# Kernel tuning notes

Measured on AMD Instinct MI355X. Metric: run time of the kernel, lower is better.

The kernel has to match this reference:

```python
import jax, jax.numpy as jnp
import numpy as np

N_NODES = 100000
N_EDGES = 3200000
NUM_GRAPHS = 512


def _glorot(key, shape):
    fan_in, fan_out = shape[0], shape[1]
    lim = float(np.sqrt(6.0 / (fan_in + fan_out)))
    return jax.random.uniform(key, shape, jnp.float32, -lim, lim)


def setup_inputs() -> dict:
    key = jax.random.key(0)
    ks = jax.random.split(key, 12)
    x = jax.random.normal(ks[0], (N_NODES, 3), jnp.float32)
    edge_index = jax.random.randint(ks[1], (2, N_EDGES), 0, N_NODES, jnp.int64)
    batch = jnp.sort(jax.random.randint(ks[2], (N_NODES,), 0, NUM_GRAPHS, jnp.int64))
    return {
        'x': x,
        'edge_index': edge_index,
        'batch': batch,
        'W1': _glorot(ks[3], (3, 32)), 'b1': jnp.zeros((32,), jnp.float32),
        'W2': _glorot(ks[4], (32, 64)), 'b2': jnp.zeros((64,), jnp.float32),
        'W3': _glorot(ks[5], (64, 64)), 'b3': jnp.zeros((64,), jnp.float32),
        'lW1': _glorot(ks[6], (64, 32)), 'lb1': jnp.zeros((32,), jnp.float32),
        'lW2': _glorot(ks[7], (32, 5)), 'lb2': jnp.zeros((5,), jnp.float32),
    }


def gcn_conv(x, src, dst, W, b, n):
    # PyG GCNConv: add self-loops, symmetric deg^{-1/2} normalization,
    # linear transform then gather-scale-scatter aggregation.
    loop = jnp.arange(n, dtype=src.dtype)
    s = jnp.concatenate([src, loop])
    d = jnp.concatenate([dst, loop])
    deg = jax.ops.segment_sum(jnp.ones_like(d, dtype=x.dtype), d, num_segments=n)
    dinv = jnp.where(deg > 0, jax.lax.rsqrt(deg), 0.0)
    norm = dinv[s] * dinv[d]  # [E+N]
    h = x @ W                 # [N, out]
    out = jax.ops.segment_sum(h[s] * norm[:, None], d, num_segments=n)
    return out + b


def reference(x, edge_index, batch, W1, b1, W2, b2, W3, b3, lW1, lb1, lW2, lb2):
    src, dst = edge_index[0], edge_index[1]
    n = x.shape[0]
    h = jax.nn.relu(gcn_conv(x, src, dst, W1, b1, n))
    h = jax.nn.relu(gcn_conv(h, src, dst, W2, b2, n))
    h = gcn_conv(h, src, dst, W3, b3, n)
    pooled = jax.ops.segment_sum(h, batch, num_segments=NUM_GRAPHS)  # [G, 64]
    z = jax.nn.relu(pooled @ lW1 + lb1)
    z = z @ lW2 + lb2
    # original applies log_softmax over dim=0 (the graph axis)
    return jax.nn.log_softmax(z, axis=0)
```

## Files before the change

### kernel.cpp

```cpp
#include <hip/hip_runtime.h>
#include <hip/hip_fp16.h>

#define N_GRAPHS 512
#define NB 1563
#define KNODE 64
#define CAP 3072
#define EPW 8192


__global__ void k_part(const int4* __restrict__ src4, const int4* __restrict__ dst4,
                       int* __restrict__ gCnt, unsigned* __restrict__ ebuf, int E4) {
    __shared__ unsigned pos[NB];
    __shared__ int dstc[EPW];
    int t = threadIdx.x;
    int e0 = blockIdx.x * (EPW / 4);
    int cnt4 = E4 - e0 < EPW / 4 ? E4 - e0 : EPW / 4;
    for (int i = t; i < NB; i += 256) pos[i] = 0;
    __syncthreads();
    for (int i = t; i < cnt4; i += 256) {
        int4 d = dst4[e0 + i];
        dstc[4 * i + 0] = d.x; dstc[4 * i + 1] = d.y;
        dstc[4 * i + 2] = d.z; dstc[4 * i + 3] = d.w;
        atomicAdd(&pos[d.x >> 6], 1u);
        atomicAdd(&pos[d.y >> 6], 1u);
        atomicAdd(&pos[d.z >> 6], 1u);
        atomicAdd(&pos[d.w >> 6], 1u);
    }
    __syncthreads();
    for (int b = t; b < NB; b += 256) {
        unsigned c = pos[b];
        unsigned base = c ? (unsigned)atomicAdd(&gCnt[b], (int)c) : 0u;
        pos[b] = (unsigned)b * CAP + base;
    }
    __syncthreads();
    for (int i = t; i < cnt4; i += 256) {
        int4 s = src4[e0 + i];
#pragma unroll
        for (int q = 0; q < 4; ++q) {
            int d = dstc[4 * i + q];
            int sv = q == 0 ? s.x : q == 1 ? s.y : q == 2 ? s.z : s.w;
            int bkt = d >> 6;
            unsigned p = atomicAdd(&pos[bkt], 1u);
            if (p < (unsigned)(bkt + 1) * CAP)
                ebuf[p] = (unsigned)sv | ((unsigned)(d & 63) << 20);
        }
    }
}


__global__ void k_csr(unsigned* __restrict__ ebuf, const int* __restrict__ gCnt,
                      int2* __restrict__ rows, float* __restrict__ dinv, int n) {
    __shared__ unsigned ec[CAP];
    __shared__ int deg[KNODE];
    __shared__ int pfx[KNODE];
    int b = blockIdx.x, t = threadIdx.x;
    int cnt = gCnt[b];
    if (cnt > CAP) cnt = CAP;
    if (t < KNODE) deg[t] = 0;
    __syncthreads();
    unsigned* eb = ebuf + (size_t)b * CAP;
    for (int i = t; i < cnt; i += 256) {
        unsigned p = eb[i];
        ec[i] = p;
        atomicAdd(&deg[p >> 20], 1);
    }
    __syncthreads();
    if (t == 0) {
        int a = 0;
        for (int i = 0; i < KNODE; ++i) { pfx[i] = a; a += deg[i]; }
    }
    __syncthreads();
    if (t < KNODE) {
        int node = b * KNODE + t;
        if (node < n) {
            rows[node] = make_int2(b * CAP + pfx[t], deg[t]);
            dinv[node] = rsqrtf((float)(deg[t] + 1));
        }
    }
    if (t < KNODE) deg[t] = pfx[t];
    __syncthreads();
    for (int i = t; i < cnt; i += 256) {
        unsigned p = ec[i];
        int pp = atomicAdd(&deg[p >> 20], 1);
        eb[pp] = p & 0xFFFFFu;
    }
}


__global__ void k_pre1(const float* __restrict__ x, const float* __restrict__ dinv,
                       float4* __restrict__ ts0, int n) {
    int i = blockIdx.x * 256 + threadIdx.x;
    if (i >= n) return;
    float d = dinv[i];
    ts0[i] = make_float4(d * x[3 * i], d * x[3 * i + 1], d * x[3 * i + 2], 0.f);
}


__global__ void k_agg1(const float4* __restrict__ ts0, const unsigned* __restrict__ esrc,
                       const int2* __restrict__ rows, const float* __restrict__ dinv,
                       float4* __restrict__ o1, int n) {
    int node = blockIdx.x * 256 + threadIdx.x;
    if (node >= n) return;
    int2 rc = rows[node];
    int s0 = rc.x, deg = rc.y;
    float4 a = ts0[node];
    int e = 0;
    for (; e + 4 <= deg; e += 4) {
        unsigned i0 = esrc[s0 + e + 0];
        unsigned i1 = esrc[s0 + e + 1];
        unsigned i2 = esrc[s0 + e + 2];
        unsigned i3 = esrc[s0 + e + 3];
        float4 v0 = ts0[i0], v1 = ts0[i1], v2 = ts0[i2], v3 = ts0[i3];
        a.x += v0.x + v1.x + v2.x + v3.x;
        a.y += v0.y + v1.y + v2.y + v3.y;
        a.z += v0.z + v1.z + v2.z + v3.z;
    }
    for (; e < deg; ++e) {
        float4 v = ts0[esrc[s0 + e]];
        a.x += v.x; a.y += v.y; a.z += v.z;
    }
    float d = dinv[node];
    o1[node] = make_float4(d * a.x, d * a.y, d * a.z, 0.f);
}


__global__ void k_t1(const float4* __restrict__ o1, const float* __restrict__ W1,
                     const float* __restrict__ b1, const float* __restrict__ dinv,
                     uint4* __restrict__ ts1, int n) {
    __shared__ float sW[96];
    __shared__ float sb[32];
    int t = threadIdx.x;
    if (t < 96) sW[t] = W1[t];
    if (t < 32) sb[t] = b1[t];
    __syncthreads();
    int ln = t >> 2, c = t & 3;
    int node = blockIdx.x * 64 + ln;
    if (node >= n) return;
    float4 o = o1[node];
    float d = dinv[node];
    float r[8];
#pragma unroll
    for (int k = 0; k < 8; ++k) {
        int j = c * 8 + k;
        float h = o.x * sW[j] + o.y * sW[32 + j] + o.z * sW[64 + j] + sb[j];
        r[k] = fmaxf(h, 0.f) * d;
    }
    __half2 h0 = __floats2half2_rn(r[0], r[1]);
    __half2 h1 = __floats2half2_rn(r[2], r[3]);
    __half2 h2 = __floats2half2_rn(r[4], r[5]);
    __half2 h3 = __floats2half2_rn(r[6], r[7]);
    uint4 w;
    w.x = *(unsigned*)&h0; w.y = *(unsigned*)&h1;
    w.z = *(unsigned*)&h2; w.w = *(unsigned*)&h3;
    ts1[(size_t)node * 4 + c] = w;
}


template <int NSLICE>
__global__ void k_aggW(const uint4* __restrict__ ts, const unsigned* __restrict__ ebuf,
                       const int* __restrict__ gCnt, const int2* __restrict__ rows,
                       const float* __restrict__ dinv, uint4* __restrict__ out, int n) {
    __shared__ unsigned eidx[CAP];
    __shared__ int cursor;
    int i = blockIdx.x;
    int b, slice;
    if (NSLICE == 1) {
        b = i; slice = 0;
    } else {
        int xcd = i & 7;
        slice = xcd & 1;
        b = (i >> 3) * 4 + (xcd >> 1);
    }
    if (b >= NB) return;
    int t = threadIdx.x;
    int cnt = gCnt[b];
    if (cnt > CAP) cnt = CAP;
    int bBase = b * CAP;
    const uint4* ebuf4 = (const uint4*)(ebuf + bBase);
    int cnt4 = (cnt + 3) >> 2;
    for (int k = t; k < cnt4; k += 128) ((uint4*)eidx)[k] = ebuf4[k];
    if (t == 0) cursor = 0;
    __syncthreads();

    const uint4* tss = ts + (size_t)slice * n * 4;
    int lane = t & 3;
    for (;;) {
        int my;
        if (lane == 0) my = atomicAdd(&cursor, 1);
        my = __shfl(my, 0, 4);
        if (my >= KNODE) break;
        int node = b * KNODE + my;
        if (node >= n) continue;
        int2 rc = rows[node];
        int ls = rc.x - bBase;
        int deg = rc.y;
        float2 a0, a1, a2, a3;
        {
            uint4 sv = tss[(size_t)node * 4 + lane];
            a0 = __half22float2(*(__half2*)&sv.x);
            a1 = __half22float2(*(__half2*)&sv.y);
            a2 = __half22float2(*(__half2*)&sv.z);
            a3 = __half22float2(*(__half2*)&sv.w);
        }
        int e = 0;
        for (; e + 4 <= deg; e += 4) {
            unsigned s0 = eidx[ls + e + 0];
            unsigned s1 = eidx[ls + e + 1];
            unsigned s2 = eidx[ls + e + 2];
            unsigned s3 = eidx[ls + e + 3];
            uint4 v0 = tss[(size_t)s0 * 4 + lane];
            uint4 v1 = tss[(size_t)s1 * 4 + lane];
            uint4 v2 = tss[(size_t)s2 * 4 + lane];
            uint4 v3 = tss[(size_t)s3 * 4 + lane];
            float2 f;
            f = __half22float2(*(__half2*)&v0.x); a0.x += f.x; a0.y += f.y;
            f = __half22float2(*(__half2*)&v0.y); a1.x += f.x; a1.y += f.y;
            f = __half22float2(*(__half2*)&v0.z); a2.x += f.x; a2.y += f.y;
            f = __half22float2(*(__half2*)&v0.w); a3.x += f.x; a3.y += f.y;
            f = __half22float2(*(__half2*)&v1.x); a0.x += f.x; a0.y += f.y;
            f = __half22float2(*(__half2*)&v1.y); a1.x += f.x; a1.y += f.y;
            f = __half22float2(*(__half2*)&v1.z); a2.x += f.x; a2.y += f.y;
            f = __half22float2(*(__half2*)&v1.w); a3.x += f.x; a3.y += f.y;
            f = __half22float2(*(__half2*)&v2.x); a0.x += f.x; a0.y += f.y;
            f = __half22float2(*(__half2*)&v2.y); a1.x += f.x; a1.y += f.y;
            f = __half22float2(*(__half2*)&v2.z); a2.x += f.x; a2.y += f.y;
            f = __half22float2(*(__half2*)&v2.w); a3.x += f.x; a3.y += f.y;
            f = __half22float2(*(__half2*)&v3.x); a0.x += f.x; a0.y += f.y;
            f = __half22float2(*(__half2*)&v3.y); a1.x += f.x; a1.y += f.y;
            f = __half22float2(*(__half2*)&v3.z); a2.x += f.x; a2.y += f.y;
            f = __half22float2(*(__half2*)&v3.w); a3.x += f.x; a3.y += f.y;
        }
        for (; e < deg; ++e) {
            unsigned s = eidx[ls + e];
            uint4 v = tss[(size_t)s * 4 + lane];
            float2 f;
            f = __half22float2(*(__half2*)&v.x); a0.x += f.x; a0.y += f.y;
            f = __half22float2(*(__half2*)&v.y); a1.x += f.x; a1.y += f.y;
            f = __half22float2(*(__half2*)&v.z); a2.x += f.x; a2.y += f.y;
            f = __half22float2(*(__half2*)&v.w); a3.x += f.x; a3.y += f.y;
        }
        float dd = dinv[node];
        __half2 o0 = __floats2half2_rn(dd * a0.x, dd * a0.y);
        __half2 o1 = __floats2half2_rn(dd * a1.x, dd * a1.y);
        __half2 o2 = __floats2half2_rn(dd * a2.x, dd * a2.y);
        __half2 o3 = __floats2half2_rn(dd * a3.x, dd * a3.y);
        uint4 w;
        w.x = *(unsigned*)&o0; w.y = *(unsigned*)&o1;
        w.z = *(unsigned*)&o2; w.w = *(unsigned*)&o3;
        out[(size_t)node * (NSLICE * 4) + slice * 4 + lane] = w;
    }
}


__global__ void k_t2(const uint4* __restrict__ o2, const float* __restrict__ W2,
                     const float* __restrict__ b2, const float* __restrict__ dinv,
                     uint4* __restrict__ ts2, int n) {
    __shared__ uint4 sO[128];
    __shared__ float sW[32 * 64];
    __shared__ float sb[64];
    int t = threadIdx.x;
    for (int i = t; i < 32 * 64; i += 256) sW[i] = W2[i];
    if (t < 64) sb[t] = b2[t];
    int node0 = blockIdx.x * 32;
    if (t < 128) {
        int nd = node0 + (t >> 2);
        sO[t] = (nd < n) ? o2[(size_t)node0 * 4 + t] : make_uint4(0, 0, 0, 0);
    }
    __syncthreads();
    int ln = t >> 3, c = t & 7;
    int node = node0 + ln;
    if (node >= n) return;
    const __half2* sOh = (const __half2*)sO;
    float acc[8];
#pragma unroll
    for (int k = 0; k < 8; ++k) acc[k] = sb[c * 8 + k];
#pragma unroll
    for (int i2 = 0; i2 < 16; ++i2) {
        float2 av = __half22float2(sOh[ln * 16 + i2]);
        const float* w0 = &sW[(2 * i2) * 64 + c * 8];
        const float* w1 = &sW[(2 * i2 + 1) * 64 + c * 8];
#pragma unroll
        for (int k = 0; k < 8; ++k) acc[k] += av.x * w0[k] + av.y * w1[k];
    }
    float d = dinv[node];
    float r[8];
#pragma unroll
    for (int k = 0; k < 8; ++k) r[k] = fmaxf(acc[k], 0.f) * d;
    __half2 h0 = __floats2half2_rn(r[0], r[1]);
    __half2 h1 = __floats2half2_rn(r[2], r[3]);
    __half2 h2 = __floats2half2_rn(r[4], r[5]);
    __half2 h3 = __floats2half2_rn(r[6], r[7]);
    uint4 w;
    w.x = *(unsigned*)&h0; w.y = *(unsigned*)&h1;
    w.z = *(unsigned*)&h2; w.w = *(unsigned*)&h3;
    ts2[((size_t)(c >> 2) * n + node) * 4 + (c & 3)] = w;
}


__global__ void k_pool(const __half2* __restrict__ h, const int* __restrict__ batch,
                       float* __restrict__ pooled, float* __restrict__ cntf, int n) {
    const int NBK = 32;
    int lane = threadIdx.x & 31;
    int sub = threadIdx.x >> 5;
    int n0 = (blockIdx.x * 8 + sub) * NBK;
    if (n0 >= n) return;
    int nend = n0 + NBK < n ? n0 + NBK : n;
    float2 acc = make_float2(0.f, 0.f);
    float rc = 0.f;
    int gcur = batch[n0];
    for (int i = n0; i < nend; ++i) {
        int g = batch[i];
        if (g != gcur) {
            atomicAdd(&pooled[gcur * 64 + 2 * lane], acc.x);
            atomicAdd(&pooled[gcur * 64 + 2 * lane + 1], acc.y);
            if (lane == 0) atomicAdd(&cntf[gcur], rc);
            acc = make_float2(0.f, 0.f);
            rc = 0.f;
            gcur = g;
        }
        float2 v = __half22float2(h[(size_t)i * 32 + lane]);
        acc.x += v.x;
        acc.y += v.y;
        rc += 1.f;
    }
    atomicAdd(&pooled[gcur * 64 + 2 * lane], acc.x);
    atomicAdd(&pooled[gcur * 64 + 2 * lane + 1], acc.y);
    if (lane == 0) atomicAdd(&cntf[gcur], rc);
}


#define GPB 4
__global__ void k_z(const float* __restrict__ P, const float* __restrict__ cntf,
                    const float* __restrict__ W3, const float* __restrict__ b3,
                    const float* __restrict__ lW1, const float* __restrict__ lb1,
                    const float* __restrict__ lW2, const float* __restrict__ lb2,
                    float* __restrict__ z) {
    __shared__ float sW3[64 * 64];
    __shared__ float sW1[64 * 32];
    __shared__ float sW2[32 * 5];
    __shared__ float sb3[64], sb1[32], sb2[5];
    __shared__ float sP[GPB][64];
    __shared__ float sH[GPB][64];
    __shared__ float sT[GPB][32];
    int t = threadIdx.x;
    for (int i = t; i < 64 * 64; i += 256) sW3[i] = W3[i];
    for (int i = t; i < 64 * 32; i += 256) sW1[i] = lW1[i];
    for (int i = t; i < 32 * 5; i += 256) sW2[i] = lW2[i];
    if (t < 64) sb3[t] = b3[t];
    if (t < 32) sb1[t] = lb1[t];
    if (t < 5) sb2[t] = lb2[t];
    int g0 = blockIdx.x * GPB;
    for (int i = t; i < GPB * 64; i += 256) sP[i >> 6][i & 63] = P[(size_t)g0 * 64 + i];
    __syncthreads();
    int lg = t >> 6;
    int j = t & 63;
    int g = g0 + lg;
    float cg = cntf[g];
    float a = cg * sb3[j];
#pragma unroll 8
    for (int i = 0; i < 64; ++i) a += sP[lg][i] * sW3[i * 64 + j];
    sH[lg][j] = a;
    __syncthreads();
    if (j < 32) {
        float a2 = sb1[j];
#pragma unroll 8
        for (int i = 0; i < 64; ++i) a2 += sH[lg][i] * sW1[i * 32 + j];
        sT[lg][j] = fmaxf(a2, 0.f);
    }
    __syncthreads();
    if (j < 5) {
        float a3 = sb2[j];
#pragma unroll
        for (int i = 0; i < 32; ++i) a3 += sT[lg][i] * sW2[i * 5 + j];
        z[g * 5 + j] = a3;
    }
}


__global__ void k_lsm(const float* __restrict__ z, float* __restrict__ out) {
    __shared__ float red[512];
    int g = threadIdx.x;
#pragma unroll
    for (int c = 0; c < 5; ++c) {
        float v = z[g * 5 + c];
        red[g] = v;
        __syncthreads();
        for (int off = 256; off > 0; off >>= 1) {
            if (g < off) red[g] = fmaxf(red[g], red[g + off]);
            __syncthreads();
        }
        float m = red[0];
        __syncthreads();
        red[g] = expf(v - m);
        __syncthreads();
        for (int off = 256; off > 0; off >>= 1) {
            if (g < off) red[g] += red[g + off];
            __syncthreads();
        }
        float lse = m + logf(red[0]);
        __syncthreads();
        out[g * 5 + c] = v - lse;
    }
}


extern "C" void kernel_launch(void* const* d_in, const int* in_sizes, int n_in,
                              void* d_out, int out_size, void* d_ws, size_t ws_size,
                              hipStream_t stream) {
    const float* x   = (const float*)d_in[0];
    const int* ei    = (const int*)d_in[1];
    const int* batch = (const int*)d_in[2];
    const float* W1  = (const float*)d_in[3];
    const float* b1  = (const float*)d_in[4];
    const float* W2  = (const float*)d_in[5];
    const float* b2  = (const float*)d_in[6];
    const float* W3  = (const float*)d_in[7];
    const float* b3  = (const float*)d_in[8];
    const float* lW1 = (const float*)d_in[9];
    const float* lb1 = (const float*)d_in[10];
    const float* lW2 = (const float*)d_in[11];
    const float* lb2 = (const float*)d_in[12];

    const int N = in_sizes[0] / 3;
    const int E = in_sizes[1] / 2;
    const int* src = ei;
    const int* dst = ei + E;

    char* ws = (char*)d_ws;
    size_t off = 0;
    auto alloc = [&](size_t bytes) -> void* {
        void* p = ws + off;
        off = (off + bytes + 255) & ~(size_t)255;
        return p;
    };

    int*      gCnt    = (int*)alloc((size_t)NB * 4);
    float*    dinv    = (float*)alloc((size_t)N * 4);
    int2*     rows    = (int2*)alloc((size_t)N * 8);
    unsigned* ebuf    = (unsigned*)alloc((size_t)NB * CAP * 4);
    float4*   ts0     = (float4*)alloc((size_t)N * 16);
    float4*   o1      = (float4*)alloc((size_t)N * 16);
    uint4*    ts1     = (uint4*)alloc((size_t)N * 4 * 16);
    uint4*    o2      = (uint4*)alloc((size_t)N * 4 * 16);
    uint4*    ts2     = (uint4*)alloc((size_t)N * 8 * 16);
    uint4*    o3      = (uint4*)alloc((size_t)N * 8 * 16);
    float*    pooledP = (float*)alloc((size_t)N_GRAPHS * 64 * 4);
    float*    cntf    = (float*)alloc((size_t)N_GRAPHS * 4);
    float*    zbuf    = (float*)alloc((size_t)N_GRAPHS * 5 * 4);

    hipMemsetAsync(gCnt, 0, (size_t)NB * 4, stream);
    hipMemsetAsync(pooledP, 0, (size_t)N_GRAPHS * 64 * 4, stream);
    hipMemsetAsync(cntf, 0, (size_t)N_GRAPHS * 4, stream);

    int nPartWg = (E + EPW - 1) / EPW;
    k_part<<<nPartWg, 256, 0, stream>>>((const int4*)src, (const int4*)dst, gCnt, ebuf, E / 4);
    k_csr<<<NB, 256, 0, stream>>>(ebuf, gCnt, rows, dinv, N);

    k_pre1<<<(N + 255) / 256, 256, 0, stream>>>(x, dinv, ts0, N);
    k_agg1<<<(N + 255) / 256, 256, 0, stream>>>(ts0, ebuf, rows, dinv, o1, N);
    k_t1<<<(N + 63) / 64, 256, 0, stream>>>(o1, W1, b1, dinv, ts1, N);

    k_aggW<1><<<NB, 128, 0, stream>>>(ts1, ebuf, gCnt, rows, dinv, o2, N);
    k_t2<<<(N + 31) / 32, 256, 0, stream>>>(o2, W2, b2, dinv, ts2, N);

    k_aggW<2><<<8 * ((NB + 3) / 4), 128, 0, stream>>>(ts2, ebuf, gCnt, rows, dinv, o3, N);

    k_pool<<<(N + 8 * 32 - 1) / (8 * 32), 256, 0, stream>>>((const __half2*)o3, batch,
                                                            pooledP, cntf, N);
    k_z<<<N_GRAPHS / GPB, 256, 0, stream>>>(pooledP, cntf, W3, b3, lW1, lb1, lW2, lb2, zbuf);
    k_lsm<<<1, 512, 0, stream>>>(zbuf, (float*)d_out);
}
```

Baseline: 245.9 us.

## Replace global-atomic bucket partition with per-chunk sort plus transposed offset table

The edge partition step no longer reserves bucket space with global atomics. Each chunk sorts its edges locally by bucket and writes them contiguously, and it records per-bucket start and count in a table. That table is transposed so each CSR block can prefix-sum the chunk offsets and gather its edges from every chunk. Workspace buffers are also aliased to reduce the memory footprint. The aim is to remove contended global atomics and scattered writes, at the cost of an extra transpose kernel and a serial per-chunk copy loop in the CSR kernel.

```diff
diff --git a/kernel.cpp b/kernel.cpp
--- a/kernel.cpp
+++ b/kernel.cpp
@@ -6,83 +6,171 @@
 #define KNODE 64
 #define CAP 3072
 #define EPW 8192
-
-
-__global__ void k_part(const int4* __restrict__ src4, const int4* __restrict__ dst4,
-                       int* __restrict__ gCnt, unsigned* __restrict__ ebuf, int E4) {
-    __shared__ unsigned pos[NB];
+#define NWMAX 400
+
+
+__global__ void k_part2(const int4* __restrict__ src4, const int4* __restrict__ dst4,
+                        unsigned* __restrict__ ebuf2, unsigned* __restrict__ P, int E, int nw) {
     __shared__ int dstc[EPW];
-    int t = threadIdx.x;
-    int e0 = blockIdx.x * (EPW / 4);
-    int cnt4 = E4 - e0 < EPW / 4 ? E4 - e0 : EPW / 4;
-    for (int i = t; i < NB; i += 256) pos[i] = 0;
-    __syncthreads();
+    __shared__ unsigned hist[NB];
+    __shared__ unsigned tsum[256];
+    int w = blockIdx.x, t = threadIdx.x;
+    int e0 = w * EPW;
+    int cnt = E - e0 < EPW ? E - e0 : EPW;
+    int cnt4 = cnt >> 2;
+    for (int i = t; i < NB; i += 256) hist[i] = 0;
+    __syncthreads();
+    const int4* d4 = dst4 + (e0 >> 2);
+    const int4* s4 = src4 + (e0 >> 2);
     for (int i = t; i < cnt4; i += 256) {
-        int4 d = dst4[e0 + i];
+        int4 d = d4[i];
         dstc[4 * i + 0] = d.x; dstc[4 * i + 1] = d.y;
         dstc[4 * i + 2] = d.z; dstc[4 * i + 3] = d.w;
-        atomicAdd(&pos[d.x >> 6], 1u);
-        atomicAdd(&pos[d.y >> 6], 1u);
-        atomicAdd(&pos[d.z >> 6], 1u);
-        atomicAdd(&pos[d.w >> 6], 1u);
-    }
-    __syncthreads();
-    for (int b = t; b < NB; b += 256) {
-        unsigned c = pos[b];
-        unsigned base = c ? (unsigned)atomicAdd(&gCnt[b], (int)c) : 0u;
-        pos[b] = (unsigned)b * CAP + base;
+        atomicAdd(&hist[d.x >> 6], 1u);
+        atomicAdd(&hist[d.y >> 6], 1u);
+        atomicAdd(&hist[d.z >> 6], 1u);
+        atomicAdd(&hist[d.w >> 6], 1u);
+    }
+    __syncthreads();
+    const int PT7 = 7;
+    unsigned loc[PT7];
+    int base = t * PT7;
+    unsigned s = 0;
+#pragma unroll
+    for (int k = 0; k < PT7; ++k) {
+        int idx = base + k;
+        unsigned v = (idx < NB) ? hist[idx] : 0u;
+        loc[k] = s;
+        s += v;
+    }
+    tsum[t] = s;
+    __syncthreads();
+    for (int off = 1; off < 256; off <<= 1) {
+        unsigned u = (t >= off) ? tsum[t - off] : 0u;
+        __syncthreads();
+        tsum[t] += u;
+        __syncthreads();
+    }
+    unsigned toff = tsum[t] - s;
+#pragma unroll
+    for (int k = 0; k < PT7; ++k) {
+        int idx = base + k;
+        if (idx < NB) {
+            unsigned cb = ((k < PT7 - 1) ? loc[k + 1] : s) - loc[k];
+            unsigned st = toff + loc[k];
+            P[(size_t)w * NB + idx] = (st << 16) | cb;
+        }
+    }
+    __syncthreads();
+#pragma unroll
+    for (int k = 0; k < PT7; ++k) {
+        int idx = base + k;
+        if (idx < NB) hist[idx] = toff + loc[k];
     }
     __syncthreads();
     for (int i = t; i < cnt4; i += 256) {
-        int4 s = src4[e0 + i];
+        int4 sv = s4[i];
 #pragma unroll
         for (int q = 0; q < 4; ++q) {
             int d = dstc[4 * i + q];
-            int sv = q == 0 ? s.x : q == 1 ? s.y : q == 2 ? s.z : s.w;
+            int svv = q == 0 ? sv.x : q == 1 ? sv.y : q == 2 ? sv.z : sv.w;
             int bkt = d >> 6;
-            unsigned p = atomicAdd(&pos[bkt], 1u);
-            if (p < (unsigned)(bkt + 1) * CAP)
-                ebuf[p] = (unsigned)sv | ((unsigned)(d & 63) << 20);
-        }
-    }
-}
-
-
-__global__ void k_csr(unsigned* __restrict__ ebuf, const int* __restrict__ gCnt,
-                      int2* __restrict__ rows, float* __restrict__ dinv, int n) {
+            unsigned pos = atomicAdd(&hist[bkt], 1u);
+            ebuf2[(size_t)e0 + pos] = (unsigned)svv | ((unsigned)(d & 63) << 20);
+        }
+    }
+}
+
+
+__global__ void kT(const unsigned* __restrict__ P, unsigned* __restrict__ PT, int nw) {
+    __shared__ unsigned tile[32][33];
+    int bw = blockIdx.x;
+    int bb = blockIdx.y;
+    int tx = threadIdx.x & 31, ty = threadIdx.x >> 5;
+#pragma unroll
+    for (int r = 0; r < 32; r += 8) {
+        int w = bw * 32 + ty + r;
+        int b = bb * 32 + tx;
+        tile[ty + r][tx] = (w < nw && b < NB) ? P[(size_t)w * NB + b] : 0u;
+    }
+    __syncthreads();
+#pragma unroll
+    for (int r = 0; r < 32; r += 8) {
+        int b = bb * 32 + ty + r;
+        int w = bw * 32 + tx;
+        if (b < NB && w < nw) PT[(size_t)b * nw + w] = tile[tx][ty + r];
+    }
+}
+
+
+__global__ void k_csr2(const unsigned* __restrict__ ebuf2, const unsigned* __restrict__ PT,
+                       unsigned* __restrict__ ebufF, int* __restrict__ gCnt,
+                       int2* __restrict__ rows, float* __restrict__ dinv, int n, int nw) {
     __shared__ unsigned ec[CAP];
-    __shared__ int deg[KNODE];
-    __shared__ int pfx[KNODE];
+    __shared__ unsigned info[NWMAX];
+    __shared__ unsigned coff[NWMAX];
+    __shared__ unsigned tsum[256];
+    __shared__ int bins[KNODE], pfx[KNODE];
     int b = blockIdx.x, t = threadIdx.x;
-    int cnt = gCnt[b];
-    if (cnt > CAP) cnt = CAP;
-    if (t < KNODE) deg[t] = 0;
-    __syncthreads();
-    unsigned* eb = ebuf + (size_t)b * CAP;
-    for (int i = t; i < cnt; i += 256) {
-        unsigned p = eb[i];
-        ec[i] = p;
-        atomicAdd(&deg[p >> 20], 1);
-    }
+    for (int w = t; w < nw; w += 256) info[w] = PT[(size_t)b * nw + w];
+    __syncthreads();
+    unsigned l0, l1, s = 0;
+    {
+        int i0 = t * 2, i1 = t * 2 + 1;
+        unsigned v0 = (i0 < nw) ? (info[i0] & 0xFFFFu) : 0u;
+        unsigned v1 = (i1 < nw) ? (info[i1] & 0xFFFFu) : 0u;
+        l0 = 0; l1 = v0; s = v0 + v1;
+    }
+    tsum[t] = s;
+    __syncthreads();
+    for (int off = 1; off < 256; off <<= 1) {
+        unsigned u = (t >= off) ? tsum[t - off] : 0u;
+        __syncthreads();
+        tsum[t] += u;
+        __syncthreads();
+    }
+    unsigned toff = tsum[t] - s;
+    {
+        int i0 = t * 2, i1 = t * 2 + 1;
+        if (i0 < nw) coff[i0] = toff + l0;
+        if (i1 < nw) coff[i1] = toff + l1;
+    }
+    __syncthreads();
+    int total = (int)tsum[255];
+    int cnt = total < CAP ? total : CAP;
+    if (t == 0) gCnt[b] = cnt;
+    for (int w = t; w < nw; w += 256) {
+        unsigned inf = info[w];
+        unsigned st = inf >> 16, c = inf & 0xFFFFu;
+        unsigned d0 = coff[w];
+        const unsigned* src = ebuf2 + (size_t)w * EPW + st;
+        for (unsigned k = 0; k < c; ++k) {
+            unsigned p = d0 + k;
+            if (p < (unsigned)CAP) ec[p] = src[k];
+        }
+    }
+    if (t < KNODE) bins[t] = 0;
+    __syncthreads();
+    for (int i = t; i < cnt; i += 256) atomicAdd(&bins[ec[i] >> 20], 1);
     __syncthreads();
     if (t == 0) {
         int a = 0;
-        for (int i = 0; i < KNODE; ++i) { pfx[i] = a; a += deg[i]; }
+        for (int i = 0; i < KNODE; ++i) { pfx[i] = a; a += bins[i]; }
     }
     __syncthreads();
     if (t < KNODE) {
         int node = b * KNODE + t;
         if (node < n) {
-            rows[node] = make_int2(b * CAP + pfx[t], deg[t]);
-            dinv[node] = rsqrtf((float)(deg[t] + 1));
-        }
-    }
-    if (t < KNODE) deg[t] = pfx[t];
+            rows[node] = make_int2(b * CAP + pfx[t], bins[t]);
+            dinv[node] = rsqrtf((float)(bins[t] + 1));
+        }
+    }
+    if (t < KNODE) bins[t] = pfx[t];
     __syncthreads();
     for (int i = t; i < cnt; i += 256) {
         unsigned p = ec[i];
-        int pp = atomicAdd(&deg[p >> 20], 1);
-        eb[pp] = p & 0xFFFFFu;
+        int pp = atomicAdd(&bins[p >> 20], 1);
+        ebufF[(size_t)b * CAP + pp] = p & 0xFFFFFu;
     }
 }
 
@@ -425,6 +513,7 @@
     const int E = in_sizes[1] / 2;
     const int* src = ei;
     const int* dst = ei + E;
+    const int nw = (E + EPW - 1) / EPW;
 
     char* ws = (char*)d_ws;
     size_t off = 0;
@@ -437,33 +526,36 @@
     int*      gCnt    = (int*)alloc((size_t)NB * 4);
     float*    dinv    = (float*)alloc((size_t)N * 4);
     int2*     rows    = (int2*)alloc((size_t)N * 8);
-    unsigned* ebuf    = (unsigned*)alloc((size_t)NB * CAP * 4);
-    float4*   ts0     = (float4*)alloc((size_t)N * 16);
-    float4*   o1      = (float4*)alloc((size_t)N * 16);
+    unsigned* ebuf2   = (unsigned*)alloc((size_t)nw * EPW * 4);
+    unsigned* P       = (unsigned*)alloc((size_t)nw * NB * 4);
+    unsigned* PT      = (unsigned*)alloc((size_t)NB * nw * 4);
+    unsigned* ebufF   = (unsigned*)alloc((size_t)NB * CAP * 4);
     uint4*    ts1     = (uint4*)alloc((size_t)N * 4 * 16);
     uint4*    o2      = (uint4*)alloc((size_t)N * 4 * 16);
     uint4*    ts2     = (uint4*)alloc((size_t)N * 8 * 16);
-    uint4*    o3      = (uint4*)alloc((size_t)N * 8 * 16);
     float*    pooledP = (float*)alloc((size_t)N_GRAPHS * 64 * 4);
     float*    cntf    = (float*)alloc((size_t)N_GRAPHS * 4);
     float*    zbuf    = (float*)alloc((size_t)N_GRAPHS * 5 * 4);
-
-    hipMemsetAsync(gCnt, 0, (size_t)NB * 4, stream);
+    float4*   ts0     = (float4*)P;
+    float4*   o1      = (float4*)PT;
+    uint4*    o3      = (uint4*)ebuf2;
+
     hipMemsetAsync(pooledP, 0, (size_t)N_GRAPHS * 64 * 4, stream);
     hipMemsetAsync(cntf, 0, (size_t)N_GRAPHS * 4, stream);
 
-    int nPartWg = (E + EPW - 1) / EPW;
-    k_part<<<nPartWg, 256, 0, stream>>>((const int4*)src, (const int4*)dst, gCnt, ebuf, E / 4);
-    k_csr<<<NB, 256, 0, stream>>>(ebuf, gCnt, rows, dinv, N);
+    k_part2<<<nw, 256, 0, stream>>>((const int4*)src, (const int4*)dst, ebuf2, P, E, nw);
+    dim3 gT((nw + 31) / 32, (NB + 31) / 32);
+    kT<<<gT, 256, 0, stream>>>(P, PT, nw);
+    k_csr2<<<NB, 256, 0, stream>>>(ebuf2, PT, ebufF, gCnt, rows, dinv, N, nw);
 
     k_pre1<<<(N + 255) / 256, 256, 0, stream>>>(x, dinv, ts0, N);
-    k_agg1<<<(N + 255) / 256, 256, 0, stream>>>(ts0, ebuf, rows, dinv, o1, N);
+    k_agg1<<<(N + 255) / 256, 256, 0, stream>>>(ts0, ebufF, rows, dinv, o1, N);
     k_t1<<<(N + 63) / 64, 256, 0, stream>>>(o1, W1, b1, dinv, ts1, N);
 
-    k_aggW<1><<<NB, 128, 0, stream>>>(ts1, ebuf, gCnt, rows, dinv, o2, N);
+    k_aggW<1><<<NB, 128, 0, stream>>>(ts1, ebufF, gCnt, rows, dinv, o2, N);
     k_t2<<<(N + 31) / 32, 256, 0, stream>>>(o2, W2, b2, dinv, ts2, N);
 
-    k_aggW<2><<<8 * ((NB + 3) / 4), 128, 0, stream>>>(ts2, ebuf, gCnt, rows, dinv, o3, N);
+    k_aggW<2><<<8 * ((NB + 3) / 4), 128, 0, stream>>>(ts2, ebufF, gCnt, rows, dinv, o3, N);
 
     k_pool<<<(N + 8 * 32 - 1) / (8 * 32), 256, 0, stream>>>((const __half2*)o3, batch,
                                                             pooledP, cntf, N);
```

After: 252.2 us. +2.6%, slower.
